# Performance work log

Measured on AMD Instinct MI355X. Metric: run time of the kernel, lower is better.

## Reference

```python
import jax, jax.numpy as jnp
import numpy as np

K = 8            # hard-coded knn k
NS = 0.2         # LeakyReLU negative slope
EPS = 1e-6
LN_EPS = 1e-5
H = 6            # num_heads


def vn_lin(W, x):
    # VNLinear: linear over vector-channel dim (axis 1). x: (B, Cin, 3, ...)
    return jnp.einsum('oc,bc...->bo...', W, x)


def vn_leaky(x, W, U):
    # VNLinearLeakyReLU (no BN): feature map p, direction map d
    p = vn_lin(W, x)
    d = vn_lin(U, x)
    dot = jnp.sum(p * d, axis=2, keepdims=True)
    dsq = jnp.sum(d * d, axis=2, keepdims=True)
    neg = p - (dot / (dsq + EPS)) * d
    return NS * p + (1.0 - NS) * jnp.where(dot >= 0, p, neg)


def vn_layernorm(x, g, b):
    # LayerNorm on per-channel vector norms, rescale directions. x: (B,C,3,N)
    n = jnp.sqrt(jnp.sum(x * x, axis=2) + EPS)            # (B,C,N)
    mu = jnp.mean(n, axis=1, keepdims=True)
    var = jnp.var(n, axis=1, keepdims=True)
    nhat = (n - mu) / jnp.sqrt(var + LN_EPS)
    nnew = g[None, :, None] * nhat + b[None, :, None]
    return x * (nnew / n)[:, :, None, :]


def vn_attention(vn_x, Wq, Wk, Wv, Wo):
    # vn_x: (B, C, 3, N); VNLinear(C, 3C) projections, multi-head SDPA over N
    B, C, _, N = vn_x.shape
    def heads(W):
        t = vn_lin(W, vn_x)                               # (B, 3C, 3, N)
        t = t.reshape(B, H, 3 * C // H, 3, N)
        return t.transpose(0, 1, 4, 2, 3).reshape(B, H, N, -1)  # (B,H,N,9C/H)
    q, k, v = heads(Wq), heads(Wk), heads(Wv)
    scale = (3 * C // H) ** -0.5                          # head_dim = dim//H = 64
    attn = jax.nn.softmax(jnp.einsum('bhqd,bhkd->bhqk', q, k) * scale, axis=-1)
    o = jnp.einsum('bhqk,bhkd->bhqd', attn, v)            # (B,H,N,9C/H)
    o = o.transpose(0, 2, 1, 3).reshape(B, N, 3 * C, 3).transpose(0, 2, 3, 1)
    return vn_lin(Wo, o)                                  # (B, C, 3, N)


def vn_get_graph_feature(x, knn_index):
    # x: (B, C, 3, N); knn_index: flat (B*K*N,) into (B*N) rows
    B, C, _, N = x.shape
    xp = x.transpose(0, 3, 1, 2).reshape(B * N, C * 3)
    feat = xp[knn_index].reshape(B, K, N, C, 3)
    xc = x.transpose(0, 3, 1, 2).reshape(B, 1, N, C, 3)
    f = jnp.concatenate([feat - xc, jnp.broadcast_to(xc, (B, K, N, C, 3))], axis=3)
    return f.transpose(0, 3, 4, 2, 1)                     # (B, 2C, 3, N, K)


def setup_inputs() -> dict:
    key = jax.random.key(0)
    ks = jax.random.split(key, 20)
    B, N, C = 4, 2048, 128
    def w(k, o, i):
        return jax.random.normal(k, (o, i), jnp.float32) * (i ** -0.5)
    return {
        'x': jax.random.normal(ks[0], (B, N, 3 * C), jnp.float32),
        'knn_index': jax.random.randint(ks[1], (B * K * N,), 0, B * N),
        'g1': jnp.ones((C,), jnp.float32), 'b1': jnp.zeros((C,), jnp.float32),
        'g2': jnp.ones((C,), jnp.float32), 'b2': jnp.zeros((C,), jnp.float32),
        'Wq': w(ks[2], 3 * C, C), 'Wk': w(ks[3], 3 * C, C), 'Wv': w(ks[4], 3 * C, C),
        'Wo': w(ks[5], C, 3 * C),
        'W1': w(ks[6], C, 2 * C), 'U1': w(ks[7], C, 2 * C),   # conv1: 256->128
        'W2': w(ks[8], C, 2 * C),                               # conv2: 256->128
        'W3': w(ks[9], 2 * C, C), 'U3': w(ks[10], 2 * C, C),   # conv3: 128->256
        'W4': w(ks[11], C, 2 * C), 'U4': w(ks[12], C, 2 * C),  # conv4: 256->128
    }


def reference(x, knn_index, g1, b1, g2, b2, Wq, Wk, Wv, Wo, W1, U1, W2, W3, U3, W4, U4):
    B, N, D = x.shape
    C = D // 3
    vn_x = x.transpose(0, 2, 1).reshape(B, C, 3, N)
    norm_x = vn_layernorm(vn_x, g1, b1)
    x_1 = vn_attention(norm_x, Wq, Wk, Wv, Wo)            # (B,C,3,N)
    knn_f = vn_get_graph_feature(norm_x, knn_index)       # (B,2C,3,N,K)
    knn_f = vn_leaky(knn_f, W1, U1)                       # (B,C,3,N,K)
    knn_f = jnp.mean(knn_f, axis=-1)                      # mean_pool over k
    x_1 = jnp.concatenate([x_1, knn_f], axis=1)           # (B,2C,3,N)
    x_1 = vn_lin(W2, x_1)                                 # (B,C,3,N)
    vn_x = vn_x + x_1
    nx2 = vn_layernorm(vn_x, g2, b2)
    h = vn_leaky(nx2, W3, U3)                             # (B,2C,3,N)
    h = vn_leaky(h, W4, U4)                               # (B,C,3,N)
    vn_x = vn_x + h
    return vn_x.reshape(B, D, N).transpose(0, 2, 1)       # (B,N,384)
```

## Files before the change

### kernel.cpp

```cpp
#include <hip/hip_runtime.h>
#include <math.h>

#define NFIX 2048
#define HH 6
#define KNN 8
#define NSLOPE 0.2f
#define EPSF 1e-6f
#define LNEPSF 1e-5f
#define QSCALE 0.18033688011112042f
#define NSPLIT 4

typedef unsigned short ushort_t;
typedef unsigned int uint_t;
typedef __attribute__((ext_vector_type(8))) short bf16x8;
typedef __attribute__((ext_vector_type(4))) short bf16x4;
typedef __attribute__((ext_vector_type(8))) _Float16 f16x8;
typedef __attribute__((ext_vector_type(4))) _Float16 f16x4;
typedef __attribute__((ext_vector_type(16))) float f32x16;
typedef __attribute__((ext_vector_type(4))) float f32x4;

__device__ __forceinline__ ushort_t f2bf(float f) {
  union { float f; unsigned u; } v; v.f = f;
  unsigned r = v.u + 0x7fff + ((v.u >> 16) & 1);
  return (ushort_t)(r >> 16);
}
__device__ __forceinline__ float bf2f(ushort_t u) {
  union { uint_t u; float f; } v; v.u = ((uint_t)u) << 16; return v.f;
}
__device__ __forceinline__ uint_t pack2(float a, float b) {
  return (uint_t)f2bf(a) | ((uint_t)f2bf(b) << 16);
}
__device__ __forceinline__ ushort_t f2h_bits(float a) {
  union { _Float16 h; ushort_t s; } cv; cv.h = (_Float16)a; return cv.s;
}
__device__ __forceinline__ uint_t packh2(float a, float b) {
  union { _Float16 h; ushort_t s; } ha, hb;
  ha.h = (_Float16)a; hb.h = (_Float16)b;
  return (uint_t)ha.s | ((uint_t)hb.s << 16);
}

__device__ __forceinline__ void vnleaky3(const float* p, const float* dv, float* out) {
  float dot = p[0]*dv[0] + p[1]*dv[1] + p[2]*dv[2];
  float dsq = dv[0]*dv[0] + dv[1]*dv[1] + dv[2]*dv[2] + EPSF;
  float f = dot / dsq;
#pragma unroll
  for (int d = 0; d < 3; ++d) {
    float neg = p[d] - f * dv[d];
    out[d] = NSLOPE * p[d] + (1.f - NSLOPE) * ((dot >= 0.f) ? p[d] : neg);
  }
}

__global__ void prep_weights(const float* __restrict__ Wq, const float* __restrict__ Wk,
                             const float* __restrict__ Wv, const float* __restrict__ Wo,
                             const float* __restrict__ W1, const float* __restrict__ U1,
                             const float* __restrict__ W2, const float* __restrict__ W3,
                             const float* __restrict__ U3, const float* __restrict__ W4,
                             const float* __restrict__ U4,
                             ushort_t* __restrict__ Wall, _Float16* __restrict__ Af16,
                             _Float16* __restrict__ W3h, _Float16* __restrict__ U3h,
                             _Float16* __restrict__ W4h, _Float16* __restrict__ U4h) {
  int idx = blockIdx.x * 256 + threadIdx.x;
  if (idx < 212992) {
    int m = idx >> 7, c = idx & 127;
    float val;
    if (m < 384)       val = Wq[m*128 + c] * QSCALE;
    else if (m < 768)  val = Wk[(m-384)*128 + c];
    else if (m < 1152) val = Wv[(m-768)*128 + c];
    else {
      int j = m - 1152;
      if (j < 128)      val = W1[j*256 + c];
      else if (j < 256) val = U1[(j-128)*256 + c];
      else if (j < 384) { int o = j-256; val = W1[o*256 + 128 + c] - W1[o*256 + c]; }
      else              { int o = j-384; val = U1[o*256 + 128 + c] - U1[o*256 + c]; }
    }
    Wall[idx] = f2bf(val); return;
  }
  idx -= 212992;
  if (idx < 49152) {
    int j = idx / 128, c = idx % 128;
    float s = 0.f;
    for (int cp = 0; cp < 128; ++cp) s += W2[c*256 + cp] * Wo[cp*384 + j];
    Af16[(size_t)c*512 + j] = (_Float16)s; return;
  }
  idx -= 49152;
  if (idx < 16384) {
    int c2 = idx / 128, c = idx % 128;
    Af16[(size_t)c*512 + 384 + c2] = (_Float16)W2[c*256 + 128 + c2]; return;
  }
  idx -= 16384;
  if (idx < 32768) { W3h[idx] = (_Float16)W3[idx]; return; }
  idx -= 32768;
  if (idx < 32768) { U3h[idx] = (_Float16)U3[idx]; return; }
  idx -= 32768;
  if (idx < 32768) { W4h[idx] = (_Float16)W4[idx]; return; }
  idx -= 32768;
  if (idx < 32768) { U4h[idx] = (_Float16)U4[idx]; return; }
}

__global__ __launch_bounds__(128) void ln1_kernel(const float* __restrict__ in,
                                                  ushort_t* __restrict__ xbp,
                                                  float* __restrict__ xdi,
                                                  const float* __restrict__ g,
                                                  const float* __restrict__ b) {
  int bn = blockIdx.x;
  int c = threadIdx.x;
  const float* row = in + (size_t)bn * 384;
  float x0 = row[c*3+0], x1 = row[c*3+1], x2 = row[c*3+2];
  float nv = sqrtf(x0*x0 + x1*x1 + x2*x2 + EPSF);
  float s1 = nv, s2 = nv*nv;
#pragma unroll
  for (int off = 32; off >= 1; off >>= 1) {
    s1 += __shfl_down(s1, off);
    s2 += __shfl_down(s2, off);
  }
  __shared__ float red[4];
  int lane = threadIdx.x & 63, w = threadIdx.x >> 6;
  if (lane == 0) { red[w*2] = s1; red[w*2+1] = s2; }
  __syncthreads();
  float tot1 = red[0] + red[2], tot2 = red[1] + red[3];
  float mu  = tot1 * (1.f/128.f);
  float var = tot2 * (1.f/128.f) - mu*mu;
  float rsig = rsqrtf(var + LNEPSF);
  float nnew = g[c] * ((nv - mu) * rsig) + b[c];
  float sc = nnew / nv;
  size_t rb = (size_t)bn * 384;
  xbp[rb + c]       = f2bf(x0*sc);
  xbp[rb + 128 + c] = f2bf(x1*sc);
  xbp[rb + 256 + c] = f2bf(x2*sc);
  xdi[rb + c]       = x0;
  xdi[rb + 128 + c] = x1;
  xdi[rb + 256 + c] = x2;
}

__global__ __launch_bounds__(128) void ln2_kernel(const float* __restrict__ in,
                                                  _Float16* __restrict__ out,
                                                  const float* __restrict__ g,
                                                  const float* __restrict__ b) {
  int bn = blockIdx.x;
  int c = threadIdx.x;
  size_t base = (size_t)bn * 384;
  float x0 = in[base + c], x1 = in[base + 128 + c], x2 = in[base + 256 + c];
  float nv = sqrtf(x0*x0 + x1*x1 + x2*x2 + EPSF);
  float s1 = nv, s2 = nv*nv;
#pragma unroll
  for (int off = 32; off >= 1; off >>= 1) {
    s1 += __shfl_down(s1, off);
    s2 += __shfl_down(s2, off);
  }
  __shared__ float red[4];
  int lane = threadIdx.x & 63, w = threadIdx.x >> 6;
  if (lane == 0) { red[w*2] = s1; red[w*2+1] = s2; }
  __syncthreads();
  float tot1 = red[0] + red[2], tot2 = red[1] + red[3];
  float mu  = tot1 * (1.f/128.f);
  float var = tot2 * (1.f/128.f) - mu*mu;
  float rsig = rsqrtf(var + LNEPSF);
  float nnew = g[c] * ((nv - mu) * rsig) + b[c];
  float sc = nnew / nv;
  out[base + c]       = (_Float16)(x0*sc);
  out[base + 128 + c] = (_Float16)(x1*sc);
  out[base + 256 + c] = (_Float16)(x2*sc);
}

#define XT_PITCH 132
#define WT_PITCH 132
#define TR_PITCH 36
__global__ __launch_bounds__(256, 2) void qkv_conv1_mfma(
    const ushort_t* __restrict__ xb, const ushort_t* __restrict__ Wall,
    ushort_t* __restrict__ q, ushort_t* __restrict__ k, ushort_t* __restrict__ v,
    _Float16* __restrict__ YZh, _Float16* __restrict__ NBh) {
  __shared__ ushort_t xs[128*XT_PITCH];
  __shared__ ushort_t wt[32*WT_PITCH];
  __shared__ float tr[4][32*TR_PITCH];
  int nb = blockIdx.x % 192;
  int mq = blockIdx.x / 192;
  int n0 = nb * 128;
  int t = threadIdx.x;
  int w = t >> 6, lane = t & 63, ql = lane & 31, hl = lane >> 5;
  for (int idx = t; idx < 2048; idx += 256) {
    int n = idx >> 4, c16 = idx & 15;
    bf16x8 gv = *(const bf16x8*)&xb[(size_t)(n0 + n)*128 + c16*8];
    ushort_t* dst = &xs[n*XT_PITCH + c16*8];
    *(bf16x4*)dst = __builtin_shufflevector(gv, gv, 0, 1, 2, 3);
    *(bf16x4*)(dst+4) = __builtin_shufflevector(gv, gv, 4, 5, 6, 7);
  }
  __syncthreads();
  bf16x8 xf[8];
  {
    const ushort_t* xr = &xs[(w*32 + ql)*XT_PITCH + hl*8];
#pragma unroll
    for (int cs = 0; cs < 8; ++cs) {
      bf16x4 lo = *(const bf16x4*)(xr + cs*16);
      bf16x4 hi = *(const bf16x4*)(xr + cs*16 + 4);
      xf[cs] = __builtin_shufflevector(lo, hi, 0, 1, 2, 3, 4, 5, 6, 7);
    }
  }
  int ng = n0 + w*32 + ql;
  int pt = ng / 3;
  int d  = ng - 3*pt;
  float* trw = tr[w];
  for (int mt = 0; mt < 13; ++mt) {
    int m0 = mq*416 + mt*32;
    __syncthreads();
    for (int idx = t; idx < 512; idx += 256) {
      int mm = idx >> 4, c16 = idx & 15;
      bf16x8 gv = *(const bf16x8*)&Wall[(size_t)(m0 + mm)*128 + c16*8];
      ushort_t* dst = &wt[mm*WT_PITCH + c16*8];
      *(bf16x4*)dst = __builtin_shufflevector(gv, gv, 0, 1, 2, 3);
      *(bf16x4*)(dst+4) = __builtin_shufflevector(gv, gv, 4, 5, 6, 7);
    }
    __syncthreads();
    f32x16 acc;
#pragma unroll
    for (int r = 0; r < 16; ++r) acc[r] = 0.f;
    const ushort_t* wr = &wt[ql*WT_PITCH + hl*8];
#pragma unroll
    for (int cs = 0; cs < 8; ++cs) {
      bf16x4 lo = *(const bf16x4*)(wr + cs*16);
      bf16x4 hi = *(const bf16x4*)(wr + cs*16 + 4);
      bf16x8 af = __builtin_shufflevector(lo, hi, 0, 1, 2, 3, 4, 5, 6, 7);
      acc = __builtin_amdgcn_mfma_f32_32x32x16_bf16(af, xf[cs], acc, 0, 0, 0);
    }
#pragma unroll
    for (int r = 0; r < 16; ++r) {
      int mrow = (r&3) + 8*(r>>2) + 4*hl;
      trw[ql*TR_PITCH + mrow] = acc[r];
    }
    asm volatile("s_waitcnt lgkmcnt(0)" ::: "memory");
    float4 c0 = *(float4*)&trw[ql*TR_PITCH + hl*16 + 0];
    float4 c1 = *(float4*)&trw[ql*TR_PITCH + hl*16 + 4];
    float4 c2 = *(float4*)&trw[ql*TR_PITCH + hl*16 + 8];
    float4 c3 = *(float4*)&trw[ql*TR_PITCH + hl*16 + 12];
    asm volatile("s_waitcnt lgkmcnt(0)" ::: "memory");
    int mg = m0 + hl*16;
    if (m0 < 1152) {
      uint4 s0, s1;
      s0.x = pack2(c0.x, c0.y); s0.y = pack2(c0.z, c0.w);
      s0.z = pack2(c1.x, c1.y); s0.w = pack2(c1.z, c1.w);
      s1.x = pack2(c2.x, c2.y); s1.y = pack2(c2.z, c2.w);
      s1.z = pack2(c3.x, c3.y); s1.w = pack2(c3.z, c3.w);
      ushort_t* dst;
      if (m0 < 384)       dst = q + (size_t)pt*1152 + d*384 + mg;
      else if (m0 < 768)  dst = k + (size_t)pt*1152 + d*384 + (mg - 384);
      else                dst = v + (size_t)pt*1152 + d*384 + (mg - 768);
      *(uint4*)dst = s0;
      *(uint4*)(dst + 8) = s1;
    } else {
      int mat = mg - 1152;
      int sub = mat >> 7, o = mat & 127;
      _Float16* basep = (sub < 2) ? YZh : NBh;
      _Float16* dst = basep + (size_t)pt*768 + d*256 + (sub & 1)*128 + o;
      uint4 s0, s1;
      s0.x = packh2(c0.x, c0.y); s0.y = packh2(c0.z, c0.w);
      s0.z = packh2(c1.x, c1.y); s0.w = packh2(c1.z, c1.w);
      s1.x = packh2(c2.x, c2.y); s1.y = packh2(c2.z, c2.w);
      s1.z = packh2(c3.x, c3.y); s1.w = packh2(c3.z, c3.w);
      *(uint4*)dst = s0;
      *(uint4*)(dst + 8) = s1;
    }
  }
}

__global__ __launch_bounds__(128) void conv1_post(const _Float16* __restrict__ YZh,
    const _Float16* __restrict__ NBh, const int* __restrict__ knn_index,
    _Float16* __restrict__ kmf16) {
  int bn = blockIdx.x;
  int b = bn / NFIX, n = bn % NFIX;
  int t = threadIdx.x;
  __shared__ int sidx[KNN];
  if (t < KNN) sidx[t] = knn_index[(b*KNN + t)*NFIX + n];
  __syncthreads();
  float yb[3], zb[3];
#pragma unroll
  for (int d = 0; d < 3; ++d) {
    yb[d] = (float)NBh[(size_t)bn*768 + d*256 + t];
    zb[d] = (float)NBh[(size_t)bn*768 + d*256 + 128 + t];
  }
  float om[3] = {0.f, 0.f, 0.f};
#pragma unroll
  for (int kk = 0; kk < KNN; ++kk) {
    const _Float16* r = YZh + (size_t)sidx[kk]*768;
    float p[3], dd[3];
#pragma unroll
    for (int d = 0; d < 3; ++d) {
      p[d]  = (float)r[d*256 + t] + yb[d];
      dd[d] = (float)r[d*256 + 128 + t] + zb[d];
    }
    float res[3];
    vnleaky3(p, dd, res);
    om[0] += res[0]; om[1] += res[1]; om[2] += res[2];
  }
#pragma unroll
  for (int d = 0; d < 3; ++d)
    kmf16[((size_t)bn*3 + d)*128 + t] = (_Float16)(om[d] * (1.f/KNN));
}

#define VT_LP 196
__global__ __launch_bounds__(256) void vtrans_kernel(const ushort_t* __restrict__ v,
                                                     ushort_t* __restrict__ vT) {
  __shared__ ushort_t tl[64*VT_LP];
  int blk = blockIdx.x;
  int bh = blk / 32, ptile = blk % 32;
  int b = bh / HH, h = bh % HH;
  int pt0 = ptile * 64;
  int t = threadIdx.x;
#pragma unroll
  for (int i = 0; i < 6; ++i) {
    int u = i*256 + t;
    int p = u / 24, seg = u % 24;
    int d = seg >> 3, c8 = seg & 7;
    bf16x8 gv = *(const bf16x8*)&v[(size_t)(b*NFIX + pt0 + p)*1152 + d*384 + h*64 + c8*8];
    ushort_t* dst = &tl[p*VT_LP + d*64 + c8*8];
    *(bf16x4*)dst = __builtin_shufflevector(gv, gv, 0, 1, 2, 3);
    *(bf16x4*)(dst+4) = __builtin_shufflevector(gv, gv, 4, 5, 6, 7);
  }
  __syncthreads();
#pragma unroll
  for (int i = 0; i < 6; ++i) {
    int u = i*256 + t;
    int ch = u >> 3, pc = u & 7;
    int ol = ch / 3, dd = ch - 3*ol;
    int cloc = dd*64 + ol;
    ushort_t hv[8];
#pragma unroll
    for (int e = 0; e < 8; ++e)
      hv[e] = tl[(pc*8 + e)*VT_LP + cloc];
    uint4 o4;
    o4.x = (uint_t)hv[0] | ((uint_t)hv[1] << 16);
    o4.y = (uint_t)hv[2] | ((uint_t)hv[3] << 16);
    o4.z = (uint_t)hv[4] | ((uint_t)hv[5] << 16);
    o4.w = (uint_t)hv[6] | ((uint_t)hv[7] << 16);
    *(uint4*)&vT[((size_t)bh*192 + ch)*2048 + pt0 + pc*8] = o4;
  }
}

#define KT_P 196
#define VT_P 36
#define TW_P 195
__global__ __launch_bounds__(256, 2) void attn_kernel(const ushort_t* __restrict__ q,
    const ushort_t* __restrict__ k, const ushort_t* __restrict__ vT,
    ushort_t* __restrict__ opart, float* __restrict__ lpart) {
  __shared__ ushort_t kt[2][32*KT_P];
  __shared__ ushort_t vt[2][192*VT_P];
  __shared__ float alds[4][32];
  int blk = blockIdx.x;
  int xcd = blk & 7, j = blk >> 3;
  int g = xcd*12 + (j >> 4);
  int qt = j & 15;
  int bh = g % 24;
  int split = g / 24;
  int b = bh / HH, h = bh % HH;
  int t = threadIdx.x;
  int w = t >> 6, lane = t & 63, ql = lane & 31, hl = lane >> 5;
  int qrow0 = qt*128 + w*32;
  const ushort_t* qpb = q + (size_t)(b*NFIX + qrow0 + ql)*1152 + h*64;
  bf16x8 qf[12];
#pragma unroll
  for (int cs = 0; cs < 12; ++cs) {
    int red0 = cs*16 + hl*8;
    int dq = red0 >> 6, ml = red0 & 63;
    qf[cs] = *(const bf16x8*)(qpb + dq*384 + ml);
  }
  const ushort_t* ksrc[3]; int kdsto[3];
  const ushort_t* vsrc[3]; int vdsto[3];
#pragma unroll
  for (int j2 = 0; j2 < 3; ++j2) {
    int idx = t + j2*256;
    int kp = idx / 24, c16 = idx % 24;
    int red0 = c16*8;
    int dk = red0 >> 6, ml = red0 & 63;
    ksrc[j2] = k + (size_t)(b*NFIX + kp)*1152 + dk*384 + h*64 + ml;
    kdsto[j2] = kp*KT_P + c16*8;
    int ch = idx >> 2, c4 = idx & 3;
    vsrc[j2] = vT + ((size_t)bh*192 + ch)*2048 + c4*8;
    vdsto[j2] = ch*VT_P + c4*8;
  }
  f32x16 acc[6];
#pragma unroll
  for (int nt = 0; nt < 6; ++nt)
#pragma unroll
    for (int r = 0; r < 16; ++r) acc[nt][r] = 0.f;
  float lsum = 0.f;
  int koff0 = split * 512;
  bf16x8 kpre[3], vpre[3];
#pragma unroll
  for (int j2 = 0; j2 < 3; ++j2) {
    kpre[j2] = *(const bf16x8*)(ksrc[j2] + (size_t)koff0*1152);
    vpre[j2] = *(const bf16x8*)(vsrc[j2] + koff0);
  }
#pragma unroll
  for (int j2 = 0; j2 < 3; ++j2) {
    ushort_t* kd = &kt[0][kdsto[j2]];
    *(bf16x4*)kd = __builtin_shufflevector(kpre[j2], kpre[j2], 0, 1, 2, 3);
    *(bf16x4*)(kd+4) = __builtin_shufflevector(kpre[j2], kpre[j2], 4, 5, 6, 7);
    ushort_t* vd = &vt[0][vdsto[j2]];
    *(bf16x4*)vd = __builtin_shufflevector(vpre[j2], vpre[j2], 0, 1, 2, 3);
    *(bf16x4*)(vd+4) = __builtin_shufflevector(vpre[j2], vpre[j2], 4, 5, 6, 7);
  }
  __syncthreads();
  for (int kb = 0; kb < 16; ++kb) {
    int cur = kb & 1;
    if (kb < 15) {
      int koff = koff0 + (kb+1)*32;
#pragma unroll
      for (int j2 = 0; j2 < 3; ++j2) {
        kpre[j2] = *(const bf16x8*)(ksrc[j2] + (size_t)koff*1152);
        vpre[j2] = *(const bf16x8*)(vsrc[j2] + koff);
      }
    }
    f32x16 sca, scb;
#pragma unroll
    for (int r = 0; r < 16; ++r) { sca[r] = 0.f; scb[r] = 0.f; }
    const ushort_t* ktc = kt[cur];
#pragma unroll
    for (int cs = 0; cs < 12; ++cs) {
      const ushort_t* kr = &ktc[ql*KT_P + cs*16 + hl*8];
      bf16x4 alo = *(const bf16x4*)kr;
      bf16x4 ahi = *(const bf16x4*)(kr + 4);
      bf16x8 af = __builtin_shufflevector(alo, ahi, 0, 1, 2, 3, 4, 5, 6, 7);
      if (cs & 1) scb = __builtin_amdgcn_mfma_f32_32x32x16_bf16(af, qf[cs], scb, 0, 0, 0);
      else        sca = __builtin_amdgcn_mfma_f32_32x32x16_bf16(af, qf[cs], sca, 0, 0, 0);
    }
    uint_t u[8], pex[8];
#pragma unroll
    for (int g2 = 0; g2 < 4; ++g2) {
      float p0 = __builtin_amdgcn_exp2f(sca[g2*4 + 0] + scb[g2*4 + 0]);
      float p1 = __builtin_amdgcn_exp2f(sca[g2*4 + 1] + scb[g2*4 + 1]);
      float p2 = __builtin_amdgcn_exp2f(sca[g2*4 + 2] + scb[g2*4 + 2]);
      float p3 = __builtin_amdgcn_exp2f(sca[g2*4 + 3] + scb[g2*4 + 3]);
      lsum += (p0 + p1) + (p2 + p3);
      u[2*g2]   = pack2(p0, p1);
      u[2*g2+1] = pack2(p2, p3);
    }
#pragma unroll
    for (int j2 = 0; j2 < 8; ++j2) pex[j2] = (uint_t)__shfl_xor((int)u[j2], 32);
    const ushort_t* vtc = vt[cur];
#pragma unroll
    for (int s = 0; s < 2; ++s) {
      uint4 au;
      au.x = hl ? pex[4*s+2] : u[4*s+0];
      au.y = hl ? pex[4*s+3] : u[4*s+1];
      au.z = hl ? u[4*s+2]   : pex[4*s+0];
      au.w = hl ? u[4*s+3]   : pex[4*s+1];
      union { uint4 ui; bf16x8 bv; } cvt; cvt.ui = au;
      bf16x8 pa = cvt.bv;
#pragma unroll
      for (int nt = 0; nt < 6; ++nt) {
        const ushort_t* vr = &vtc[(nt*32 + ql)*VT_P + s*16 + hl*8];
        bf16x4 vlo = *(const bf16x4*)vr;
        bf16x4 vhi = *(const bf16x4*)(vr + 4);
        bf16x8 vf = __builtin_shufflevector(vlo, vhi, 0, 1, 2, 3, 4, 5, 6, 7);
        acc[nt] = __builtin_amdgcn_mfma_f32_32x32x16_bf16(pa, vf, acc[nt], 0, 0, 0);
      }
    }
    if (kb < 15) {
      int nxt = cur ^ 1;
#pragma unroll
      for (int j2 = 0; j2 < 3; ++j2) {
        ushort_t* kd = &kt[nxt][kdsto[j2]];
        *(bf16x4*)kd = __builtin_shufflevector(kpre[j2], kpre[j2], 0, 1, 2, 3);
        *(bf16x4*)(kd+4) = __builtin_shufflevector(kpre[j2], kpre[j2], 4, 5, 6, 7);
        ushort_t* vd = &vt[nxt][vdsto[j2]];
        *(bf16x4*)vd = __builtin_shufflevector(vpre[j2], vpre[j2], 0, 1, 2, 3);
        *(bf16x4*)(vd+4) = __builtin_shufflevector(vpre[j2], vpre[j2], 4, 5, 6, 7);
      }
    }
    __syncthreads();
  }
  lsum += __shfl_xor(lsum, 32);
  if (lane < 32) {
    alds[w][ql] = 1.0f / lsum;
    lpart[(size_t)split*24*NFIX + (size_t)bh*NFIX + qrow0 + ql] = lsum;
  }
  asm volatile("s_waitcnt lgkmcnt(0)" ::: "memory");
  float lv[4][4];
#pragma unroll
  for (int g2 = 0; g2 < 4; ++g2) {
    f32x4 tv = *(const f32x4*)&alds[w][8*g2 + 4*hl];
#pragma unroll
    for (int rr = 0; rr < 4; ++rr) lv[g2][rr] = tv[rr];
  }
  ushort_t* tw = (w == 0) ? kt[0] : (w == 1) ? kt[1] : (w == 2) ? vt[0] : vt[1];
#pragma unroll
  for (int nt = 0; nt < 6; ++nt) {
    int ch = nt*32 + ql;
#pragma unroll
    for (int r = 0; r < 16; ++r) {
      int qrow = (r&3) + 8*(r>>2) + 4*hl;
      tw[qrow*TW_P + ch] = f2h_bits(acc[nt][r] * lv[r>>2][r&3]);
    }
  }
  asm volatile("s_waitcnt lgkmcnt(0)" ::: "memory");
  const size_t SS = (size_t)8192*1152;
  ushort_t* opb = opart + (size_t)split*SS;
  size_t nbase = (size_t)(b*NFIX + qrow0) * 3;
#pragma unroll
  for (int i = 0; i < 12; ++i) {
    int chunk = i*64 + lane;
    int nl = chunk >> 3, jc = chunk & 7;
    int qq = nl / 3, dd = nl - 3*qq;
    ushort_t hv[8];
#pragma unroll
    for (int e = 0; e < 8; ++e)
      hv[e] = tw[qq*TW_P + (jc*8 + e)*3 + dd];
    uint4 sv;
    sv.x = (uint_t)hv[0] | ((uint_t)hv[1] << 16);
    sv.y = (uint_t)hv[2] | ((uint_t)hv[3] << 16);
    sv.z = (uint_t)hv[4] | ((uint_t)hv[5] << 16);
    sv.w = (uint_t)hv[6] | ((uint_t)hv[7] << 16);
    *(uint4*)&opb[(nbase + nl)*384 + h*64 + jc*8] = sv;
  }
}

#define AP 68
__global__ __launch_bounds__(384) void x1mid_mfma(
    const float* __restrict__ xdi, const ushort_t* __restrict__ opart,
    const float* __restrict__ lpart, const _Float16* __restrict__ kmf16,
    const _Float16* __restrict__ Af16, float* __restrict__ xmid) {
  __shared__ __align__(16) char smem[33536];
  _Float16* As = (_Float16*)smem;
  _Float16* Bt = (_Float16*)(smem + 17408);
  float* wlsL  = (float*)(smem + 30464);
  float* trbase = (float*)smem;
  int blk = blockIdx.x;
  int n0 = blk * 96;
  int pt0 = blk * 32;
  int t = threadIdx.x;
  int w = t >> 6, lane = t & 63, ql = lane & 31, hl = lane >> 5;
  int nsub = w >> 1, mh = w & 1;
  if (t < 192) {
    int ptl = t / 6, h = t % 6;
    int ptg = pt0 + ptl;
    int b = ptg >> 11, n = ptg & 2047;
    size_t lidx = (size_t)(b*HH + h)*NFIX + n;
    float l[NSPLIT]; float tot = 0.f;
#pragma unroll
    for (int s = 0; s < NSPLIT; ++s) {
      l[s] = lpart[(size_t)s*24*NFIX + lidx];
      tot += l[s];
    }
    float rd = 1.f / tot;
    float* wp = &wlsL[(ptl*6 + h)*NSPLIT];
#pragma unroll
    for (int s = 0; s < NSPLIT; ++s) wp[s] = l[s]*rd;
  }
  f32x16 acc[2];
#pragma unroll
  for (int m2 = 0; m2 < 2; ++m2)
#pragma unroll
    for (int r = 0; r < 16; ++r) acc[m2][r] = 0.f;
  const size_t SS = (size_t)8192*1152;
  __syncthreads();
  for (int p = 0; p < 8; ++p) {
    for (int u = t; u < 1024; u += 384) {
      int m = u >> 3, kc = u & 7;
      f16x4 a0 = *(const f16x4*)&Af16[(size_t)m*512 + p*64 + kc*8];
      f16x4 a1 = *(const f16x4*)&Af16[(size_t)m*512 + p*64 + kc*8 + 4];
      _Float16* dst = &As[m*AP + kc*8];
      *(f16x4*)dst = a0;
      *(f16x4*)(dst+4) = a1;
    }
    {
      int u = t;
      if (u < 384) {
        int n_l = u >> 2, jc = u & 3;
        int n_g = n0 + n_l;
        _Float16* dst = &Bt[n_l*AP + jc*16];
        if (p < 6) {
          int pt_l = n_l / 3;
          const float* wp = &wlsL[(pt_l*6 + p)*NSPLIT];
          float facc[16];
#pragma unroll
          for (int e = 0; e < 16; ++e) facc[e] = 0.f;
#pragma unroll
          for (int s = 0; s < NSPLIT; ++s) {
            const ushort_t* src = opart + s*SS + (size_t)n_g*384 + p*64 + jc*16;
            uint4 ra = *(const uint4*)src;
            uint4 rb = *(const uint4*)(src + 8);
            const _Float16* ua = (const _Float16*)&ra;
            const _Float16* ub = (const _Float16*)&rb;
            float wsc = wp[s];
#pragma unroll
            for (int e = 0; e < 8; ++e) {
              facc[e]     += wsc * (float)ua[e];
              facc[8 + e] += wsc * (float)ub[e];
            }
          }
          _Float16 hv[16];
#pragma unroll
          for (int e = 0; e < 16; ++e) hv[e] = (_Float16)facc[e];
#pragma unroll
          for (int g = 0; g < 4; ++g)
            *(f16x4*)(dst + g*4) = *(f16x4*)&hv[g*4];
        } else {
          const _Float16* src = kmf16 + (size_t)n_g*128 + (p-6)*64 + jc*16;
          f16x4 v0 = *(const f16x4*)src;
          f16x4 v1 = *(const f16x4*)(src + 4);
          f16x4 v2 = *(const f16x4*)(src + 8);
          f16x4 v3 = *(const f16x4*)(src + 12);
          *(f16x4*)dst = v0; *(f16x4*)(dst+4) = v1;
          *(f16x4*)(dst+8) = v2; *(f16x4*)(dst+12) = v3;
        }
      }
    }
    __syncthreads();
#pragma unroll
    for (int cs = 0; cs < 4; ++cs) {
      int kloc = cs*16 + hl*8;
      f16x4 b0 = *(const f16x4*)&Bt[(nsub*32 + ql)*AP + kloc];
      f16x4 b1 = *(const f16x4*)&Bt[(nsub*32 + ql)*AP + kloc + 4];
      f16x8 bf = __builtin_shufflevector(b0, b1, 0, 1, 2, 3, 4, 5, 6, 7);
#pragma unroll
      for (int m2 = 0; m2 < 2; ++m2) {
        int mrow = (mh*2 + m2)*32 + ql;
        f16x4 a0 = *(const f16x4*)&As[mrow*AP + kloc];
        f16x4 a1 = *(const f16x4*)&As[mrow*AP + kloc + 4];
        f16x8 af = __builtin_shufflevector(a0, a1, 0, 1, 2, 3, 4, 5, 6, 7);
        acc[m2] = __builtin_amdgcn_mfma_f32_32x32x16_f16(af, bf, acc[m2], 0, 0, 0);
      }
    }
    __syncthreads();
  }
  float* trw = trbase + w*32*34;
#pragma unroll
  for (int m2 = 0; m2 < 2; ++m2) {
#pragma unroll
    for (int r = 0; r < 16; ++r) {
      int mrow = (r&3) + 8*(r>>2) + 4*hl;
      trw[ql*34 + mrow] = acc[m2][r];
    }
    asm volatile("s_waitcnt lgkmcnt(0)" ::: "memory");
    float4 c0 = *(float4*)&trw[ql*34 + hl*16 + 0];
    float4 c1 = *(float4*)&trw[ql*34 + hl*16 + 4];
    float4 c2 = *(float4*)&trw[ql*34 + hl*16 + 8];
    float4 c3 = *(float4*)&trw[ql*34 + hl*16 + 12];
    asm volatile("s_waitcnt lgkmcnt(0)" ::: "memory");
    int n_g = n0 + nsub*32 + ql;
    int c0g = (mh*2 + m2)*32 + hl*16;
    const float* xd = xdi + (size_t)n_g*128 + c0g;
    float4 x0 = *(const float4*)xd;
    float4 x1 = *(const float4*)(xd + 4);
    float4 x2 = *(const float4*)(xd + 8);
    float4 x3 = *(const float4*)(xd + 12);
    c0.x += x0.x; c0.y += x0.y; c0.z += x0.z; c0.w += x0.w;
    c1.x += x1.x; c1.y += x1.y; c1.z += x1.z; c1.w += x1.w;
    c2.x += x2.x; c2.y += x2.y; c2.z += x2.z; c2.w += x2.w;
    c3.x += x3.x; c3.y += x3.y; c3.z += x3.z; c3.w += x3.w;
    float* dst = xmid + (size_t)n_g*128 + c0g;
    *(float4*)dst = c0;
    *(float4*)(dst + 4) = c1;
    *(float4*)(dst + 8) = c2;
    *(float4*)(dst + 12) = c3;
  }
}

#define X3P 132
#define TR3P 36
__global__ __launch_bounds__(256) void conv3_mfma(const _Float16* __restrict__ nxh,
    const _Float16* __restrict__ W3h, const _Float16* __restrict__ U3h,
    _Float16* __restrict__ h3) {
  __shared__ __align__(16) _Float16 Xs[3*32*X3P];
  __shared__ __align__(16) _Float16 tr3[4][96*TR3P];
  int blk = blockIdx.x;
  int pt0 = (blk >> 1) * 32;
  int oh = blk & 1;
  int t = threadIdx.x;
  int w = t >> 6, lane = t & 63, ql = lane & 31, hl = lane >> 5;
#pragma unroll
  for (int i = 0; i < 6; ++i) {
    int u = i*256 + t;
    int r = u >> 4, c8 = u & 15;
    f16x8 gv = *(const f16x8*)&nxh[(size_t)(pt0*3 + r)*128 + c8*8];
    int d = r % 3, p = r / 3;
    _Float16* dst = &Xs[(d*32 + p)*X3P + c8*8];
    *(f16x4*)dst = __builtin_shufflevector(gv, gv, 0, 1, 2, 3);
    *(f16x4*)(dst+4) = __builtin_shufflevector(gv, gv, 4, 5, 6, 7);
  }
  __syncthreads();
  int ot = oh*128 + w*32;
  const _Float16* Wp = W3h + (size_t)(ot + ql)*128 + hl*8;
  const _Float16* Up = U3h + (size_t)(ot + ql)*128 + hl*8;
  f32x16 accP[3], accD[3];
#pragma unroll
  for (int d = 0; d < 3; ++d)
#pragma unroll
    for (int r = 0; r < 16; ++r) { accP[d][r] = 0.f; accD[d][r] = 0.f; }
#pragma unroll
  for (int cs = 0; cs < 8; ++cs) {
    f16x8 wf = *(const f16x8*)(Wp + cs*16);
    f16x8 uf = *(const f16x8*)(Up + cs*16);
#pragma unroll
    for (int d = 0; d < 3; ++d) {
      const _Float16* xr = &Xs[(d*32 + ql)*X3P + cs*16 + hl*8];
      f16x4 lo = *(const f16x4*)xr;
      f16x4 hi = *(const f16x4*)(xr + 4);
      f16x8 xf = __builtin_shufflevector(lo, hi, 0, 1, 2, 3, 4, 5, 6, 7);
      accP[d] = __builtin_amdgcn_mfma_f32_32x32x16_f16(wf, xf, accP[d], 0, 0, 0);
      accD[d] = __builtin_amdgcn_mfma_f32_32x32x16_f16(uf, xf, accD[d], 0, 0, 0);
    }
  }
  _Float16* trw = tr3[w];
#pragma unroll
  for (int r = 0; r < 16; ++r) {
    int olr = (r&3) + 8*(r>>2) + 4*hl;
    float p3[3], d3[3], res[3];
#pragma unroll
    for (int d = 0; d < 3; ++d) { p3[d] = accP[d][r]; d3[d] = accD[d][r]; }
    vnleaky3(p3, d3, res);
#pragma unroll
    for (int d = 0; d < 3; ++d) trw[(ql*3 + d)*TR3P + olr] = (_Float16)res[d];
  }
  asm volatile("s_waitcnt lgkmcnt(0)" ::: "memory");
#pragma unroll
  for (int i = 0; i < 6; ++i) {
    int u = i*64 + lane;
    int row = u >> 2, c8 = u & 3;
    const _Float16* src = &trw[row*TR3P + c8*8];
    f16x4 lo = *(const f16x4*)src;
    f16x4 hi = *(const f16x4*)(src + 4);
    f16x8 ov = __builtin_shufflevector(lo, hi, 0, 1, 2, 3, 4, 5, 6, 7);
    *(f16x8*)&h3[(size_t)(pt0*3 + row)*256 + ot + c8*8] = ov;
  }
}

#define X4P 260
#define TF4P 388
__global__ __launch_bounds__(256) void conv4_mfma(const _Float16* __restrict__ h3,
    const _Float16* __restrict__ W4h, const _Float16* __restrict__ U4h,
    const float* __restrict__ xmid, float* __restrict__ out) {
  __shared__ __align__(16) _Float16 Xs[3*16*X4P];
  __shared__ __align__(16) float trF[16*TF4P];
  int pt0 = blockIdx.x * 16;
  int t = threadIdx.x;
  int w = t >> 6, lane = t & 63;
  int nl = lane & 15, kq = lane >> 4;
#pragma unroll
  for (int i = 0; i < 6; ++i) {
    int u = i*256 + t;
    int r = u >> 5, c8 = u & 31;
    f16x8 gv = *(const f16x8*)&h3[(size_t)(pt0*3 + r)*256 + c8*8];
    int d = r % 3, p = r / 3;
    _Float16* dst = &Xs[(d*16 + p)*X4P + c8*8];
    *(f16x4*)dst = __builtin_shufflevector(gv, gv, 0, 1, 2, 3);
    *(f16x4*)(dst+4) = __builtin_shufflevector(gv, gv, 4, 5, 6, 7);
  }
  __syncthreads();
  int ot = w*32;
  f32x4 accP[2][3], accD[2][3];
#pragma unroll
  for (int mt = 0; mt < 2; ++mt)
#pragma unroll
    for (int d = 0; d < 3; ++d)
#pragma unroll
      for (int r = 0; r < 4; ++r) { accP[mt][d][r] = 0.f; accD[mt][d][r] = 0.f; }
  const _Float16* Wb = W4h + (size_t)ot*256;
  const _Float16* Ub = U4h + (size_t)ot*256;
#pragma unroll
  for (int cs = 0; cs < 8; ++cs) {
    int kof = cs*32 + kq*8;
    f16x8 xf[3];
#pragma unroll
    for (int d = 0; d < 3; ++d) {
      const _Float16* xr = &Xs[(d*16 + nl)*X4P + kof];
      f16x4 lo = *(const f16x4*)xr;
      f16x4 hi = *(const f16x4*)(xr + 4);
      xf[d] = __builtin_shufflevector(lo, hi, 0, 1, 2, 3, 4, 5, 6, 7);
    }
#pragma unroll
    for (int mt = 0; mt < 2; ++mt) {
      f16x8 wf = *(const f16x8*)(Wb + (size_t)(mt*16 + nl)*256 + kof);
      f16x8 uf = *(const f16x8*)(Ub + (size_t)(mt*16 + nl)*256 + kof);
#pragma unroll
      for (int d = 0; d < 3; ++d) {
        accP[mt][d] = __builtin_amdgcn_mfma_f32_16x16x32_f16(wf, xf[d], accP[mt][d], 0, 0, 0);
        accD[mt][d] = __builtin_amdgcn_mfma_f32_16x16x32_f16(uf, xf[d], accD[mt][d], 0, 0, 0);
      }
    }
  }
#pragma unroll
  for (int mt = 0; mt < 2; ++mt)
#pragma unroll
    for (int r = 0; r < 4; ++r) {
      int o = ot + mt*16 + kq*4 + r;
      float p3[3], d3[3], res[3];
#pragma unroll
      for (int d = 0; d < 3; ++d) { p3[d] = accP[mt][d][r]; d3[d] = accD[mt][d][r]; }
      vnleaky3(p3, d3, res);
#pragma unroll
      for (int d = 0; d < 3; ++d) trF[nl*TF4P + o*3 + d] = res[d];
    }
  __syncthreads();
#pragma unroll
  for (int i = 0; i < 6; ++i) {
    int u = i*256 + t;
    int row = u / 96, c4 = u % 96;
    float4 vv = *(float4*)&trF[row*TF4P + c4*4];
    int bn = pt0 + row;
    float rs[4];
    const float* fv = (const float*)&vv;
#pragma unroll
    for (int e = 0; e < 4; ++e) {
      int col = c4*4 + e;
      int o = col / 3, d = col - 3*o;
      rs[e] = fv[e] + xmid[(size_t)(3*bn + d)*128 + o];
    }
    float4 ov; ov.x = rs[0]; ov.y = rs[1]; ov.z = rs[2]; ov.w = rs[3];
    *(float4*)&out[(size_t)bn*384 + c4*4] = ov;
  }
}

extern "C" void kernel_launch(void* const* d_in, const int* in_sizes, int n_in,
                              void* d_out, int out_size, void* d_ws, size_t ws_size,
                              hipStream_t stream) {
  const float* x   = (const float*)d_in[0];
  const int* knn   = (const int*)d_in[1];
  const float* g1  = (const float*)d_in[2];
  const float* b1  = (const float*)d_in[3];
  const float* g2  = (const float*)d_in[4];
  const float* b2  = (const float*)d_in[5];
  const float* Wq  = (const float*)d_in[6];
  const float* Wk  = (const float*)d_in[7];
  const float* Wv  = (const float*)d_in[8];
  const float* Wo  = (const float*)d_in[9];
  const float* W1  = (const float*)d_in[10];
  const float* U1  = (const float*)d_in[11];
  const float* W2  = (const float*)d_in[12];
  const float* W3  = (const float*)d_in[13];
  const float* U3  = (const float*)d_in[14];
  const float* W4  = (const float*)d_in[15];
  const float* U4  = (const float*)d_in[16];
  float* out = (float*)d_out;
  (void)n_in; (void)out_size; (void)ws_size;

  const size_t BN = (size_t)in_sizes[0] / 384;

  float* ws    = (float*)d_ws;
  float* xdi   = ws;
  float* xmid  = xdi + BN*384;
  _Float16* kmf16 = (_Float16*)(xmid + BN*384);
  ushort_t* xbp = (ushort_t*)(kmf16 + BN*384);
  ushort_t* qb = xbp + BN*384;
  ushort_t* kb = qb + BN*1152;
  ushort_t* vb = kb + BN*1152;
  ushort_t* vT = vb + BN*1152;
  ushort_t* Wall = vT + BN*1152;
  _Float16* Af16 = (_Float16*)(Wall + 212992);
  _Float16* W3h = Af16 + 65536;
  _Float16* U3h = W3h + 32768;
  _Float16* W4h = U3h + 32768;
  _Float16* U4h = W4h + 32768;
  ushort_t* opart = (ushort_t*)(U4h + 32768);
  float* lpart = (float*)(opart + 4*BN*1152);
  _Float16* YZh = (_Float16*)opart;
  _Float16* NBh = YZh + BN*768;
  _Float16* nxh = (_Float16*)qb;
  _Float16* h3  = (_Float16*)kb;

  prep_weights<<<1600, 256, 0, stream>>>(Wq, Wk, Wv, Wo, W1, U1, W2, W3, U3, W4, U4,
                                         Wall, Af16, W3h, U3h, W4h, U4h);
  ln1_kernel<<<(int)BN, 128, 0, stream>>>(x, xbp, xdi, g1, b1);
  qkv_conv1_mfma<<<192*4, 256, 0, stream>>>(xbp, Wall, qb, kb, vb, YZh, NBh);
  conv1_post<<<(int)BN, 128, 0, stream>>>(YZh, NBh, knn, kmf16);
  vtrans_kernel<<<768, 256, 0, stream>>>(vb, vT);
  attn_kernel<<<16*24*NSPLIT, 256, 0, stream>>>(qb, kb, vT, opart, lpart);
  x1mid_mfma<<<256, 384, 0, stream>>>(xdi, opart, lpart, kmf16, Af16, xmid);
  ln2_kernel<<<(int)BN, 128, 0, stream>>>(xmid, nxh, g2, b2);
  conv3_mfma<<<512, 256, 0, stream>>>(nxh, W3h, U3h, h3);
  conv4_mfma<<<512, 256, 0, stream>>>(h3, W4h, U4h, xmid, out);
}
```

Measured before the change: 337.5 us.

## Fuse second layernorm into x1mid epilogue and halve attention key splits

Removes the standalone ln2 kernel. The x1mid MFMA kernel now stages its residual-added output tile in shared memory, computes per-point vector-norm statistics there, and writes the normalized fp16 input for conv3 directly, saving a launch and a round trip of xmid through global memory. Attention split-K drops from 4 to 2, so each block walks 1024 keys and fewer partial outputs need combining, at the cost of fewer blocks and less parallelism. The larger shared-memory footprint in x1mid may reduce occupancy, and the combine step must still agree with NSPLIT.

```diff
diff --git a/kernel.cpp b/kernel.cpp
--- a/kernel.cpp
+++ b/kernel.cpp
@@ -8,7 +8,7 @@
 #define EPSF 1e-6f
 #define LNEPSF 1e-5f
 #define QSCALE 0.18033688011112042f
-#define NSPLIT 4
+#define NSPLIT 2
 
 typedef unsigned short ushort_t;
 typedef unsigned int uint_t;
@@ -130,36 +130,6 @@
   xdi[rb + c]       = x0;
   xdi[rb + 128 + c] = x1;
   xdi[rb + 256 + c] = x2;
-}
-
-__global__ __launch_bounds__(128) void ln2_kernel(const float* __restrict__ in,
-                                                  _Float16* __restrict__ out,
-                                                  const float* __restrict__ g,
-                                                  const float* __restrict__ b) {
-  int bn = blockIdx.x;
-  int c = threadIdx.x;
-  size_t base = (size_t)bn * 384;
-  float x0 = in[base + c], x1 = in[base + 128 + c], x2 = in[base + 256 + c];
-  float nv = sqrtf(x0*x0 + x1*x1 + x2*x2 + EPSF);
-  float s1 = nv, s2 = nv*nv;
-#pragma unroll
-  for (int off = 32; off >= 1; off >>= 1) {
-    s1 += __shfl_down(s1, off);
-    s2 += __shfl_down(s2, off);
-  }
-  __shared__ float red[4];
-  int lane = threadIdx.x & 63, w = threadIdx.x >> 6;
-  if (lane == 0) { red[w*2] = s1; red[w*2+1] = s2; }
-  __syncthreads();
-  float tot1 = red[0] + red[2], tot2 = red[1] + red[3];
-  float mu  = tot1 * (1.f/128.f);
-  float var = tot2 * (1.f/128.f) - mu*mu;
-  float rsig = rsqrtf(var + LNEPSF);
-  float nnew = g[c] * ((nv - mu) * rsig) + b[c];
-  float sc = nnew / nv;
-  out[base + c]       = (_Float16)(x0*sc);
-  out[base + 128 + c] = (_Float16)(x1*sc);
-  out[base + 256 + c] = (_Float16)(x2*sc);
 }
 
 #define XT_PITCH 132
@@ -345,7 +315,7 @@
   __shared__ float alds[4][32];
   int blk = blockIdx.x;
   int xcd = blk & 7, j = blk >> 3;
-  int g = xcd*12 + (j >> 4);
+  int g = xcd*6 + (j >> 4);
   int qt = j & 15;
   int bh = g % 24;
   int split = g / 24;
@@ -381,7 +351,7 @@
 #pragma unroll
     for (int r = 0; r < 16; ++r) acc[nt][r] = 0.f;
   float lsum = 0.f;
-  int koff0 = split * 512;
+  int koff0 = split * 1024;
   bf16x8 kpre[3], vpre[3];
 #pragma unroll
   for (int j2 = 0; j2 < 3; ++j2) {
@@ -398,9 +368,9 @@
     *(bf16x4*)(vd+4) = __builtin_shufflevector(vpre[j2], vpre[j2], 4, 5, 6, 7);
   }
   __syncthreads();
-  for (int kb = 0; kb < 16; ++kb) {
+  for (int kb = 0; kb < 32; ++kb) {
     int cur = kb & 1;
-    if (kb < 15) {
+    if (kb < 31) {
       int koff = koff0 + (kb+1)*32;
 #pragma unroll
       for (int j2 = 0; j2 < 3; ++j2) {
@@ -453,7 +423,7 @@
         acc[nt] = __builtin_amdgcn_mfma_f32_32x32x16_bf16(pa, vf, acc[nt], 0, 0, 0);
       }
     }
-    if (kb < 15) {
+    if (kb < 31) {
       int nxt = cur ^ 1;
 #pragma unroll
       for (int j2 = 0; j2 < 3; ++j2) {
@@ -513,15 +483,19 @@
 }
 
 #define AP 68
+#define XLP 132
 __global__ __launch_bounds__(384) void x1mid_mfma(
     const float* __restrict__ xdi, const ushort_t* __restrict__ opart,
     const float* __restrict__ lpart, const _Float16* __restrict__ kmf16,
-    const _Float16* __restrict__ Af16, float* __restrict__ xmid) {
-  __shared__ __align__(16) char smem[33536];
+    const _Float16* __restrict__ Af16, float* __restrict__ xmid,
+    _Float16* __restrict__ nxh, const float* __restrict__ g2,
+    const float* __restrict__ b2) {
+  __shared__ __align__(16) char smem[50944];
   _Float16* As = (_Float16*)smem;
   _Float16* Bt = (_Float16*)(smem + 17408);
   float* wlsL  = (float*)(smem + 30464);
-  float* trbase = (float*)smem;
+  float* X     = (float*)smem;
+  float* stats = (float*)(smem + 50688);
   int blk = blockIdx.x;
   int n0 = blk * 96;
   int pt0 = blk * 32;
@@ -621,36 +595,75 @@
     }
     __syncthreads();
   }
-  float* trw = trbase + w*32*34;
 #pragma unroll
   for (int m2 = 0; m2 < 2; ++m2) {
+    int cbase = (mh*2 + m2)*32 + 4*hl;
+    float* xrow = &X[(nsub*32 + ql)*XLP];
 #pragma unroll
     for (int r = 0; r < 16; ++r) {
-      int mrow = (r&3) + 8*(r>>2) + 4*hl;
-      trw[ql*34 + mrow] = acc[m2][r];
-    }
-    asm volatile("s_waitcnt lgkmcnt(0)" ::: "memory");
-    float4 c0 = *(float4*)&trw[ql*34 + hl*16 + 0];
-    float4 c1 = *(float4*)&trw[ql*34 + hl*16 + 4];
-    float4 c2 = *(float4*)&trw[ql*34 + hl*16 + 8];
-    float4 c3 = *(float4*)&trw[ql*34 + hl*16 + 12];
-    asm volatile("s_waitcnt lgkmcnt(0)" ::: "memory");
-    int n_g = n0 + nsub*32 + ql;
-    int c0g = (mh*2 + m2)*32 + hl*16;
-    const float* xd = xdi + (size_t)n_g*128 + c0g;
-    float4 x0 = *(const float4*)xd;
-    float4 x1 = *(const float4*)(xd + 4);
-    float4 x2 = *(const float4*)(xd + 8);
-    float4 x3 = *(const float4*)(xd + 12);
-    c0.x += x0.x; c0.y += x0.y; c0.z += x0.z; c0.w += x0.w;
-    c1.x += x1.x; c1.y += x1.y; c1.z += x1.z; c1.w += x1.w;
-    c2.x += x2.x; c2.y += x2.y; c2.z += x2.z; c2.w += x2.w;
-    c3.x += x3.x; c3.y += x3.y; c3.z += x3.z; c3.w += x3.w;
-    float* dst = xmid + (size_t)n_g*128 + c0g;
-    *(float4*)dst = c0;
-    *(float4*)(dst + 4) = c1;
-    *(float4*)(dst + 8) = c2;
-    *(float4*)(dst + 12) = c3;
+      int col = cbase + (r&3) + 8*(r>>2);
+      xrow[col] = acc[m2][r];
+    }
+  }
+  __syncthreads();
+#pragma unroll
+  for (int i = 0; i < 4; ++i) {
+    int u = i*384 + t;
+    int row = u >> 4, c0 = (u & 15) * 8;
+    float* xp = &X[row*XLP + c0];
+    const float* xd = xdi + (size_t)(n0 + row)*128 + c0;
+    float4 a0 = *(float4*)xp, a1 = *(float4*)(xp + 4);
+    float4 d0 = *(const float4*)xd, d1 = *(const float4*)(xd + 4);
+    a0.x += d0.x; a0.y += d0.y; a0.z += d0.z; a0.w += d0.w;
+    a1.x += d1.x; a1.y += d1.y; a1.z += d1.z; a1.w += d1.w;
+    *(float4*)xp = a0; *(float4*)(xp + 4) = a1;
+    float* dst = xmid + (size_t)(n0 + row)*128 + c0;
+    *(float4*)dst = a0; *(float4*)(dst + 4) = a1;
+  }
+  __syncthreads();
+  for (int pi = w; pi < 32; pi += 6) {
+    int c = lane;
+    float a0 = X[(pi*3+0)*XLP + c], a1 = X[(pi*3+1)*XLP + c], a2 = X[(pi*3+2)*XLP + c];
+    float e0 = X[(pi*3+0)*XLP + c + 64], e1 = X[(pi*3+1)*XLP + c + 64], e2 = X[(pi*3+2)*XLP + c + 64];
+    float nva = sqrtf(a0*a0 + a1*a1 + a2*a2 + EPSF);
+    float nvb = sqrtf(e0*e0 + e1*e1 + e2*e2 + EPSF);
+    float s1 = nva + nvb;
+    float s2 = nva*nva + nvb*nvb;
+#pragma unroll
+    for (int off = 32; off >= 1; off >>= 1) {
+      s1 += __shfl_down(s1, off);
+      s2 += __shfl_down(s2, off);
+    }
+    if (lane == 0) {
+      float mu = s1 * (1.f/128.f);
+      float var = s2 * (1.f/128.f) - mu*mu;
+      stats[pi*2]   = mu;
+      stats[pi*2+1] = rsqrtf(var + LNEPSF);
+    }
+  }
+  __syncthreads();
+#pragma unroll
+  for (int i = 0; i < 4; ++i) {
+    int u = i*384 + t;
+    int row = u >> 4, c0 = (u & 15) * 8;
+    int pt_l = row / 3;
+    float mu = stats[pt_l*2], rsig = stats[pt_l*2+1];
+    const float* r0 = &X[(pt_l*3 + 0)*XLP + c0];
+    const float* r1 = &X[(pt_l*3 + 1)*XLP + c0];
+    const float* r2 = &X[(pt_l*3 + 2)*XLP + c0];
+    const float* rd = &X[row*XLP + c0];
+    float xv[8];
+#pragma unroll
+    for (int e = 0; e < 8; ++e) {
+      float x0 = r0[e], x1 = r1[e], x2 = r2[e];
+      float nv = sqrtf(x0*x0 + x1*x1 + x2*x2 + EPSF);
+      float nnew = g2[c0 + e] * ((nv - mu) * rsig) + b2[c0 + e];
+      xv[e] = rd[e] * (nnew / nv);
+    }
+    uint4 sv;
+    sv.x = packh2(xv[0], xv[1]); sv.y = packh2(xv[2], xv[3]);
+    sv.z = packh2(xv[4], xv[5]); sv.w = packh2(xv[6], xv[7]);
+    *(uint4*)&nxh[(size_t)(n0 + row)*128 + c0] = sv;
   }
 }
 
@@ -863,8 +876,7 @@
   conv1_post<<<(int)BN, 128, 0, stream>>>(YZh, NBh, knn, kmf16);
   vtrans_kernel<<<768, 256, 0, stream>>>(vb, vT);
   attn_kernel<<<16*24*NSPLIT, 256, 0, stream>>>(qb, kb, vT, opart, lpart);
-  x1mid_mfma<<<256, 384, 0, stream>>>(xdi, opart, lpart, kmf16, Af16, xmid);
-  ln2_kernel<<<(int)BN, 128, 0, stream>>>(xmid, nxh, g2, b2);
+  x1mid_mfma<<<256, 384, 0, stream>>>(xdi, opart, lpart, kmf16, Af16, xmid, nxh, g2, b2);
   conv3_mfma<<<512, 256, 0, stream>>>(nxh, W3h, U3h, h3);
   conv4_mfma<<<512, 256, 0, stream>>>(h3, W4h, U4h, xmid, out);
 }
```

Measured after the change: 329.3 us. -2.4%, faster.
